# Performance work log

Hardware: AMD Instinct MI355X
Metric: run time of the kernel (lower is better)

The kernel has to match this reference:

```python
import jax, jax.numpy as jnp
from jax import lax
import numpy as np

N_STATE, N_CTRL, T, B = 64, 32, 50, 256
N = N_STATE + N_CTRL


def setup_inputs() -> dict:
    key = jax.random.key(0)
    k1, k2, k3, k4, k5, k6 = jax.random.split(key, 6)
    # SPD cost Hessians so Qt_uu stays invertible through the Riccati recursion
    A = jax.random.normal(k1, (T, B, N, N), jnp.float32) / np.float32(np.sqrt(N))
    C = jnp.einsum('tbij,tbkj->tbik', A, A) + jnp.eye(N, dtype=jnp.float32)
    c = 0.1 * jax.random.normal(k2, (T, B, N), jnp.float32)
    # mildly contractive dynamics to keep the 50-step recursion well-scaled
    F = jax.random.normal(k3, (T, B, N_STATE, N), jnp.float32) * np.float32(0.5 / np.sqrt(N))
    x_init = jax.random.normal(k4, (B, N_STATE), jnp.float32)
    current_x = jax.random.normal(k5, (T, B, N_STATE), jnp.float32)
    current_u = jax.random.normal(k6, (T, B, N_CTRL), jnp.float32)
    return {'x_init': x_init, 'C': C, 'c': c, 'F': F,
            'current_x': current_x, 'current_u': current_u}


def _lqr(x_init, C, c, F, current_x, current_u):
    ns = current_x.shape[-1]
    # delta_space linearized cost: c_back[t] = C[t] @ [x_t; u_t] + c[t]
    xut = jnp.concatenate([current_x, current_u], axis=-1)          # [T,B,N]
    c_back = jnp.einsum('tbij,tbj->tbi', C, xut) + c                # [T,B,N]

    def bwd_step(carry, inp):
        V, v = carry                                                # [B,ns,ns],[B,ns]
        Ct, ct, Ft = inp
        FtT = jnp.swapaxes(Ft, -1, -2)                              # [B,N,ns]
        Qt = Ct + FtT @ V @ Ft                                      # [B,N,N]
        qt = ct + jnp.einsum('bij,bi->bj', Ft, v)                   # Ft^T v
        Q_xx = Qt[:, :ns, :ns]; Q_xu = Qt[:, :ns, ns:]
        Q_ux = Qt[:, ns:, :ns]; Q_uu = Qt[:, ns:, ns:]
        q_x = qt[:, :ns]; q_u = qt[:, ns:]
        Kt = -jnp.linalg.solve(Q_uu, Q_ux)                          # [B,nc,ns]
        kt = -jnp.linalg.solve(Q_uu, q_u[..., None])[..., 0]        # [B,nc]
        KtT = jnp.swapaxes(Kt, -1, -2)
        Vn = Q_xx + Q_xu @ Kt + KtT @ Q_ux + KtT @ Q_uu @ Kt
        vn = (q_x + jnp.einsum('bij,bj->bi', Q_xu, kt)
              + jnp.einsum('bji,bj->bi', Kt, q_u)
              + jnp.einsum('bji,bjk,bk->bi', Kt, Q_uu, kt))
        return (Vn, vn), (Kt, kt)

    Bsz = x_init.shape[0]
    V0 = jnp.zeros((Bsz, ns, ns), C.dtype)
    v0 = jnp.zeros((Bsz, ns), C.dtype)
    # scan from t = T-1 down to 0 (V0 = 0 makes the last step Qt = C[T-1])
    _, (K_rev, k_rev) = lax.scan(bwd_step, (V0, v0),
                                 (C[::-1], c_back[::-1], F[::-1]))
    K = K_rev[::-1]   # [T,B,nc,ns], gain at time t
    k = k_rev[::-1]   # [T,B,nc]

    # forward rollout (single line-search iter, alpha = 1)
    x_ref_next = jnp.concatenate([current_x[1:], jnp.zeros_like(current_x[:1])], 0)

    def fwd_step(carry, inp):
        xt, dxt = carry
        Kt, kt, ut, Ft, xr = inp
        new_ut = jnp.einsum('bij,bj->bi', Kt, dxt) + ut + kt
        new_xut = jnp.concatenate([xt, new_ut], axis=-1)
        x_next = jnp.einsum('bij,bj->bi', Ft, new_xut)
        return (x_next, x_next - xr), (xt, new_ut)

    _, (new_x, new_u) = lax.scan(fwd_step, (x_init, jnp.zeros_like(x_init)),
                                 (K, k, current_u, F, x_ref_next))
    return new_x, new_u


def reference(x_init, C, c, F, current_x, current_u):
    return _lqr(x_init, C, c, F, current_x, current_u)
```

## Files before the change

### kernel.cpp

```cpp
#include <hip/hip_runtime.h>
#include <cstddef>

#define NS 64
#define NC 32
#define NN 96
#define TT 50
#define BB 256
#define NT 512

#define VS 68
#define QS 104
#define FS 104
#define AS 104

#define OFF_V    0
#define OFF_Q    4352
#define OFF_F    14336
#define OFF_M    20992
#define OFF_A    27648
#define OFF_PR   30976
#define OFF_PC   31808
#define OFF_XUT  32064
#define OFF_CV   32160
#define OFF_QT   32256
#define OFF_VV   32352
#define LDS_FLOATS 32416

__device__ __forceinline__ void bar() {
    asm volatile("s_waitcnt lgkmcnt(0)\n\ts_barrier" ::: "memory");
}

__device__ __forceinline__ float frcp(float x) {
    float r = __builtin_amdgcn_rcpf(x);
    return r * (2.f - x * r);
}

extern "C" __global__ __launch_bounds__(NT, 1)
void lqr_fused(const float* __restrict__ x_init,
               const float* __restrict__ Cg, const float* __restrict__ cg,
               const float* __restrict__ Fg, const float* __restrict__ cxg,
               const float* __restrict__ cug, float* __restrict__ Kg,
               float* __restrict__ kg, float* __restrict__ out)
{
    extern __shared__ float sm[];
    float* Vb   = sm + OFF_V;
    float* Qb   = sm + OFF_Q;
    float* Fb   = sm + OFF_F;
    float* Mb   = sm + OFF_M;
    float* Ab   = sm + OFF_A;
    float* PRb  = sm + OFF_PR;
    float* PCb  = sm + OFF_PC;
    float* xut  = sm + OFF_XUT;
    float* cv   = sm + OFF_CV;
    float* qtv  = sm + OFF_QT;
    float* vv   = sm + OFF_VV;

    const int b   = blockIdx.x;
    const int tid = threadIdx.x;

    float4 creg[5];
    float4 fnew[3];
    float  xreg = 0.f, cvreg = 0.f;

    {
        const int t = TT - 1;
        const float* Fsrc = Fg + ((size_t)t * BB + b) * (NS * NN);
        #pragma unroll
        for (int rr = 0; rr < 3; ++rr) {
            int f = tid + NT * rr;
            float4 val = ((const float4*)Fsrc)[f];
            int row = f / 24, c4 = f % 24;
            *(float4*)&Fb[row * FS + 4 * c4] = val;
        }
        const float* Csrc = Cg + ((size_t)t * BB + b) * (NN * NN);
        #pragma unroll
        for (int rr = 0; rr < 4; ++rr) creg[rr] = ((const float4*)Csrc)[tid + NT * rr];
        if (tid < 256) creg[4] = ((const float4*)Csrc)[tid + 2048];

        if (tid < NN) {
            xut[tid] = (tid < NS) ? cxg[((size_t)t * BB + b) * NS + tid]
                                  : cug[((size_t)t * BB + b) * NC + (tid - NS)];
            cv[tid] = cg[((size_t)t * BB + b) * NN + tid];
        }
        for (int e = tid; e < NS * VS; e += NT) Vb[e] = 0.f;
        if (tid < NS) vv[tid] = 0.f;
    }
    bar();

    for (int t = TT - 1; t >= 0; --t) {
        #pragma unroll
        for (int rr = 0; rr < 5; ++rr) {
            if (rr < 4 || tid < 256) {
                int f = tid + NT * rr;
                int row = f / 24, c4 = f % 24;
                *(float4*)&Qb[row * QS + 4 * c4] = creg[rr];
            }
        }
        if (t > 0) {
            const float* Cs = Cg + ((size_t)(t - 1) * BB + b) * (NN * NN);
            #pragma unroll
            for (int rr = 0; rr < 4; ++rr) creg[rr] = ((const float4*)Cs)[tid + NT * rr];
            if (tid < 256) creg[4] = ((const float4*)Cs)[tid + 2048];
            const float* Fs = Fg + ((size_t)(t - 1) * BB + b) * (NS * NN);
            #pragma unroll
            for (int rr = 0; rr < 3; ++rr) fnew[rr] = ((const float4*)Fs)[tid + NT * rr];
            if (tid < NN) {
                xreg  = (tid < NS) ? cxg[((size_t)(t - 1) * BB + b) * NS + tid]
                                   : cug[((size_t)(t - 1) * BB + b) * NC + (tid - NS)];
                cvreg = cg[((size_t)(t - 1) * BB + b) * NN + tid];
            }
        }

        {
            const int ty = tid >> 4, tx = tid & 15;
            const int i0 = 2 * ty, j0 = 6 * tx;
            float acc[2][6];
            #pragma unroll
            for (int a = 0; a < 2; ++a)
                #pragma unroll
                for (int q = 0; q < 6; ++q) acc[a][q] = 0.f;
            for (int k = 0; k < NS; k += 4) {
                float4 v0 = *(const float4*)&Vb[i0 * VS + k];
                float4 v1 = *(const float4*)&Vb[(i0 + 1) * VS + k];
                #pragma unroll
                for (int dk = 0; dk < 4; ++dk) {
                    float2 f0 = *(const float2*)&Fb[(k + dk) * FS + j0];
                    float2 f1 = *(const float2*)&Fb[(k + dk) * FS + j0 + 2];
                    float2 f2 = *(const float2*)&Fb[(k + dk) * FS + j0 + 4];
                    float fv[6] = {f0.x, f0.y, f1.x, f1.y, f2.x, f2.y};
                    float a0k = (&v0.x)[dk], a1k = (&v1.x)[dk];
                    #pragma unroll
                    for (int q = 0; q < 6; ++q) {
                        acc[0][q] += a0k * fv[q];
                        acc[1][q] += a1k * fv[q];
                    }
                }
            }
            #pragma unroll
            for (int a = 0; a < 2; ++a) {
                *(float2*)&Mb[(i0 + a) * FS + j0]     = make_float2(acc[a][0], acc[a][1]);
                *(float2*)&Mb[(i0 + a) * FS + j0 + 2] = make_float2(acc[a][2], acc[a][3]);
                *(float2*)&Mb[(i0 + a) * FS + j0 + 4] = make_float2(acc[a][4], acc[a][5]);
            }
        }
        bar();

        if (tid < 384) {
            const int j = tid >> 2, s = tid & 3;
            float acc = (s == 0) ? cv[j] : 0.f;
            #pragma unroll 4
            for (int it = 0; it < 24; ++it) {
                int i = 4 * it + s;
                acc += Qb[i * QS + j] * xut[i];
            }
            #pragma unroll 4
            for (int it = 0; it < 16; ++it) {
                int i = 4 * it + s;
                acc += Fb[i * FS + j] * vv[i];
            }
            acc += __shfl_down(acc, 1);
            acc += __shfl_down(acc, 2);
            if (s == 0) {
                qtv[j] = acc;
                if (j >= NS) Ab[(j - NS) * AS + 96] = acc;
            }
        }
        bar();

        {
            const int ty = tid >> 4, tx = tid & 15;
            const int a0 = 3 * ty, b0 = 6 * tx;
            float acc[3][6];
            #pragma unroll
            for (int dr = 0; dr < 3; ++dr) {
                float2 q0 = *(const float2*)&Qb[(a0 + dr) * QS + b0];
                float2 q1 = *(const float2*)&Qb[(a0 + dr) * QS + b0 + 2];
                float2 q2 = *(const float2*)&Qb[(a0 + dr) * QS + b0 + 4];
                acc[dr][0] = q0.x; acc[dr][1] = q0.y; acc[dr][2] = q1.x;
                acc[dr][3] = q1.y; acc[dr][4] = q2.x; acc[dr][5] = q2.y;
            }
            for (int i = 0; i < NS; ++i) {
                float fa0 = Fb[i * FS + a0];
                float fa1 = Fb[i * FS + a0 + 1];
                float fa2 = Fb[i * FS + a0 + 2];
                float2 m0 = *(const float2*)&Mb[i * FS + b0];
                float2 m1 = *(const float2*)&Mb[i * FS + b0 + 2];
                float2 m2 = *(const float2*)&Mb[i * FS + b0 + 4];
                float mb[6] = {m0.x, m0.y, m1.x, m1.y, m2.x, m2.y};
                float fa[3] = {fa0, fa1, fa2};
                #pragma unroll
                for (int dr = 0; dr < 3; ++dr)
                    #pragma unroll
                    for (int q = 0; q < 6; ++q) acc[dr][q] += fa[dr] * mb[q];
            }
            #pragma unroll
            for (int dr = 0; dr < 3; ++dr) {
                *(float2*)&Qb[(a0 + dr) * QS + b0]     = make_float2(acc[dr][0], acc[dr][1]);
                *(float2*)&Qb[(a0 + dr) * QS + b0 + 2] = make_float2(acc[dr][2], acc[dr][3]);
                *(float2*)&Qb[(a0 + dr) * QS + b0 + 4] = make_float2(acc[dr][4], acc[dr][5]);
                int row = a0 + dr;
                if (row >= NS) {
                    int rr = row - NS;
                    #pragma unroll
                    for (int q = 0; q < 6; ++q) {
                        int c  = b0 + q;
                        int ac = (c < NS) ? (c + NC) : (c - NS);
                        Ab[rr * AS + ac] = acc[dr][q];
                    }
                }
            }
        }
        bar();

        if (t > 0) {
            #pragma unroll
            for (int rr = 0; rr < 3; ++rr) {
                int f = tid + NT * rr;
                int row = f / 24, c4 = f % 24;
                *(float4*)&Fb[row * FS + 4 * c4] = fnew[rr];
            }
            if (tid < NN) { xut[tid] = xreg; cv[tid] = cvreg; }
        }

        float myinv = 0.f;
        {
            const int g = tid & 15, r = tid >> 4;
            const int jlo = 6 * g;
            float a[6], a6;
            #pragma unroll
            for (int q = 0; q < 6; ++q) a[q] = Ab[r * AS + jlo + q];
            a6 = (g == 15) ? Ab[r * AS + 96] : 0.f;
            if (r < 4) {
                #pragma unroll
                for (int q = 0; q < 6; ++q) PRb[r * 104 + jlo + q] = a[q];
                if (g == 15) PRb[r * 104 + 96] = a6;
            }
            if (g == 0) {
                #pragma unroll
                for (int i = 0; i < 4; ++i) PCb[i * 32 + r] = a[i];
            }
            bar();

            for (int rnd = 0; rnd < 8; ++rnd) {
                const int p0 = 4 * rnd;
                const float* PRc = PRb + (rnd & 1) * 416;
                const float* PCc = PCb + (rnd & 1) * 128;
                float* PRn = PRb + ((rnd + 1) & 1) * 416;
                float* PCn = PCb + ((rnd + 1) & 1) * 128;

                float W0p0 = PRc[0 * 104 + p0 + 0];
                float W0p1 = PRc[0 * 104 + p0 + 1];
                float W0p2 = PRc[0 * 104 + p0 + 2];
                float W0p3 = PRc[0 * 104 + p0 + 3];
                float R1p1 = PRc[1 * 104 + p0 + 1];
                float R1p2 = PRc[1 * 104 + p0 + 2];
                float R1p3 = PRc[1 * 104 + p0 + 3];
                float R2p2 = PRc[2 * 104 + p0 + 2];
                float R2p3 = PRc[2 * 104 + p0 + 3];
                float R3p3 = PRc[3 * 104 + p0 + 3];
                float C0p1 = PCc[0 * 32 + p0 + 1];
                float C0p2 = PCc[0 * 32 + p0 + 2];
                float C0p3 = PCc[0 * 32 + p0 + 3];
                float C1p2 = PCc[1 * 32 + p0 + 2];
                float C1p3 = PCc[1 * 32 + p0 + 3];
                float C2p3 = PCc[2 * 32 + p0 + 3];

                float r0 = frcp(W0p0);
                float g1 = C0p1 * r0;
                float W1p1 = R1p1 - g1 * W0p1;
                float r1 = frcp(W1p1);
                float W1p2 = R1p2 - g1 * W0p2;
                float W1p3 = R1p3 - g1 * W0p3;
                float h0 = C0p2 * r0;
                float h1 = (C1p2 - h0 * W0p1) * r1;
                float W2p2 = R2p2 - h0 * W0p2 - h1 * W1p2;
                float r2 = frcp(W2p2);
                float W2p3 = R2p3 - h0 * W0p3 - h1 * W1p3;
                float k0 = C0p3 * r0;
                float k1 = (C1p3 - k0 * W0p1) * r1;
                float k2 = (C2p3 - k0 * W0p2 - k1 * W1p2) * r2;
                float W3p3 = R3p3 - k0 * W0p3 - k1 * W1p3 - k2 * W2p3;
                float r3 = frcp(W3p3);

                float c0 = PCc[0 * 32 + r];
                float c1 = PCc[1 * 32 + r];
                float c2 = PCc[2 * 32 + r];
                float c3 = PCc[3 * 32 + r];
                float fac0 = (r == p0)     ? 0.f : c0 * r0;
                float a1   = c1 - fac0 * W0p1;
                float fac1 = (r == p0 + 1) ? 0.f : a1 * r1;
                float a2   = c2 - fac0 * W0p2 - fac1 * W1p2;
                float fac2 = (r == p0 + 2) ? 0.f : a2 * r2;
                float a3   = c3 - fac0 * W0p3 - fac1 * W1p3 - fac2 * W2p3;
                float fac3 = (r == p0 + 3) ? 0.f : a3 * r3;

                if (r == p0)     myinv = r0;
                if (r == p0 + 1) myinv = r1;
                if (r == p0 + 2) myinv = r2;
                if (r == p0 + 3) myinv = r3;

                #pragma unroll
                for (int q = 0; q < 6; ++q) {
                    float w0  = PRc[0 * 104 + jlo + q];
                    float w1r = PRc[1 * 104 + jlo + q];
                    float w2r = PRc[2 * 104 + jlo + q];
                    float w3r = PRc[3 * 104 + jlo + q];
                    float w1 = w1r - g1 * w0;
                    float w2 = w2r - h0 * w0 - h1 * w1;
                    float w3 = w3r - k0 * w0 - k1 * w1 - k2 * w2;
                    a[q] -= fac0 * w0;
                    a[q] -= fac1 * w1;
                    a[q] -= fac2 * w2;
                    a[q] -= fac3 * w3;
                }
                if (g == 15) {
                    float w0  = PRc[0 * 104 + 96];
                    float w1 = PRc[1 * 104 + 96] - g1 * w0;
                    float w2 = PRc[2 * 104 + 96] - h0 * w0 - h1 * w1;
                    float w3 = PRc[3 * 104 + 96] - k0 * w0 - k1 * w1 - k2 * w2;
                    a6 -= fac0 * w0;
                    a6 -= fac1 * w1;
                    a6 -= fac2 * w2;
                    a6 -= fac3 * w3;
                }

                if (rnd < 7) {
                    const int np0 = p0 + 4;
                    if (r >= np0 && r < np0 + 4) {
                        float* dst = PRn + (r - np0) * 104;
                        #pragma unroll
                        for (int q = 0; q < 6; ++q) dst[jlo + q] = a[q];
                        if (g == 15) dst[96] = a6;
                    }
                    #pragma unroll
                    for (int q = 0; q < 6; ++q) {
                        int c = jlo + q;
                        if (c >= np0 && c < np0 + 4) PCn[(c - np0) * 32 + r] = a[q];
                    }
                    bar();
                }
            }
            #pragma unroll
            for (int q = 0; q < 6; ++q) {
                int j = jlo + q;
                if (j >= NC) Ab[r * AS + j] = -a[q] * myinv;
            }
            if (g == 15) Ab[r * AS + 96] = -a6 * myinv;
        }
        bar();

        {
            float* Kt = Kg + ((size_t)t * BB + b) * (NC * NS);
            for (int e = tid; e < NC * NS; e += NT) {
                int m = e >> 6, x = e & 63;
                Kt[e] = Ab[m * AS + 32 + x];
            }
            if (tid < NC) kg[((size_t)t * BB + b) * NC + tid] = Ab[tid * AS + 96];
        }
        {
            const int ty = tid >> 4, tx = tid & 15;
            const int i0 = 2 * ty, j0 = 4 * tx;
            float acc[2][4];
            #pragma unroll
            for (int di = 0; di < 2; ++di) {
                float4 q = *(const float4*)&Qb[(i0 + di) * QS + j0];
                acc[di][0] = q.x; acc[di][1] = q.y; acc[di][2] = q.z; acc[di][3] = q.w;
            }
            for (int m = 0; m < NC; ++m) {
                float2 qx = *(const float2*)&Qb[(NS + m) * QS + i0];
                float4 kk = *(const float4*)&Ab[m * AS + 32 + j0];
                float kv[4] = {kk.x, kk.y, kk.z, kk.w};
                #pragma unroll
                for (int dj = 0; dj < 4; ++dj) {
                    acc[0][dj] += qx.x * kv[dj];
                    acc[1][dj] += qx.y * kv[dj];
                }
            }
            #pragma unroll
            for (int di = 0; di < 2; ++di)
                *(float4*)&Vb[(i0 + di) * VS + j0] =
                    make_float4(acc[di][0], acc[di][1], acc[di][2], acc[di][3]);
        }
        if (tid < NS) {
            float s0 = qtv[tid], s1 = 0.f;
            for (int m = 0; m < NC; m += 2) {
                s0 += Qb[(NS + m) * QS + tid] * Ab[m * AS + 96];
                s1 += Qb[(NS + m + 1) * QS + tid] * Ab[(m + 1) * AS + 96];
            }
            vv[tid] = s0 + s1;
        }
        bar();
    }

    asm volatile("s_waitcnt vmcnt(0)" ::: "memory");
    __syncthreads();

    {
        float* xpp = sm;
        float* dxs = sm + 192;
        float* out_x = out;
        float* out_u = out + (size_t)TT * BB * NS;

        if (tid < NS) { xpp[tid] = x_init[(size_t)b * NS + tid]; dxs[tid] = 0.f; }
        bar();

        const int mK = tid >> 3, qK = tid & 7;
        const int iF = tid >> 2, qF = tid & 3;
        float kr[8], fr[24];
        if (tid < 256) {
            const float* Ksrc = Kg + (size_t)b * (NC * NS);
            #pragma unroll
            for (int xx = 0; xx < 8; ++xx) kr[xx] = Ksrc[mK * NS + qK + 8 * xx];
            const float* Fsrc = Fg + (size_t)b * (NS * NN);
            #pragma unroll
            for (int jj = 0; jj < 24; ++jj) fr[jj] = Fsrc[iF * NN + qF + 4 * jj];
        }

        for (int t = 0; t < TT; ++t) {
            const int cur = (t & 1) * 96, nxt = ((t + 1) & 1) * 96;
            const int curd = (t & 1) * 64, nxtd = ((t + 1) & 1) * 64;
            float krn[8], frn[24];
            if (tid < 256) {
                int tn = (t + 1 < TT) ? (t + 1) : t;
                const float* Ksrc = Kg + ((size_t)tn * BB + b) * (NC * NS);
                #pragma unroll
                for (int xx = 0; xx < 8; ++xx) krn[xx] = Ksrc[mK * NS + qK + 8 * xx];
                const float* Fsrc = Fg + ((size_t)tn * BB + b) * (NS * NN);
                #pragma unroll
                for (int jj = 0; jj < 24; ++jj) frn[jj] = Fsrc[iF * NN + qF + 4 * jj];
            }
            if (tid < NS) out_x[((size_t)t * BB + b) * NS + tid] = xpp[cur + tid];
            if (tid < 256) {
                float s = 0.f;
                #pragma unroll
                for (int xx = 0; xx < 8; ++xx) s += kr[xx] * dxs[curd + qK + 8 * xx];
                s += __shfl_down(s, 4); s += __shfl_down(s, 2); s += __shfl_down(s, 1);
                if (qK == 0) {
                    float un = s + cug[((size_t)t * BB + b) * NC + mK]
                                 + kg[((size_t)t * BB + b) * NC + mK];
                    xpp[cur + NS + mK] = un;
                    out_u[((size_t)t * BB + b) * NC + mK] = un;
                }
            }
            bar();
            if (tid < 256) {
                float s = 0.f;
                #pragma unroll
                for (int jj = 0; jj < 24; ++jj) s += fr[jj] * xpp[cur + qF + 4 * jj];
                s += __shfl_down(s, 2); s += __shfl_down(s, 1);
                if (qF == 0) {
                    float xr = (t + 1 < TT) ? cxg[((size_t)(t + 1) * BB + b) * NS + iF] : 0.f;
                    xpp[nxt + iF] = s;
                    dxs[nxtd + iF] = s - xr;
                }
                #pragma unroll
                for (int xx = 0; xx < 8; ++xx) kr[xx] = krn[xx];
                #pragma unroll
                for (int jj = 0; jj < 24; ++jj) fr[jj] = frn[jj];
            }
            bar();
        }
    }
}

extern "C" void kernel_launch(void* const* d_in, const int* in_sizes, int n_in,
                              void* d_out, int out_size, void* d_ws, size_t ws_size,
                              hipStream_t stream)
{
    const float* x_init = (const float*)d_in[0];
    const float* Cg     = (const float*)d_in[1];
    const float* cg     = (const float*)d_in[2];
    const float* Fg     = (const float*)d_in[3];
    const float* cxg    = (const float*)d_in[4];
    const float* cug    = (const float*)d_in[5];
    float* out = (float*)d_out;

    float* Kg = (float*)d_ws;
    float* kg = Kg + (size_t)TT * BB * NC * NS;

    hipFuncSetAttribute((const void*)lqr_fused,
                        hipFuncAttributeMaxDynamicSharedMemorySize,
                        LDS_FLOATS * 4);

    lqr_fused<<<BB, NT, LDS_FLOATS * 4, stream>>>(x_init, Cg, cg, Fg, cxg, cug,
                                                  Kg, kg, out);
}
```

Measured before the change: 1.907 ms.

## Restructure Riccati step with warp-specialized phases, bigger register tiles, skipped pivot work

The backward Riccati step is reorganized in several ways. The V·F matmul now runs on 192 threads with 4x8 tiles, concurrently with the qt reduction on other threads, which removes one barrier. The FᵀM update uses 8x6 tiles with float4 loads and vectorized Ab writes, and the Gauss-Jordan elimination remaps threads so that groups whose columns are already eliminated skip work. It also vectorizes the K store, widens the V update tiles, moves the Q reload to the end of the step, and prefetches the per-step scalars in the forward rollout. The larger tiles raise register pressure and idle part of the block, and the reordered barriers risk correctness hazards.

```diff
diff --git a/kernel.cpp b/kernel.cpp
--- a/kernel.cpp
+++ b/kernel.cpp
@@ -76,18 +76,6 @@
         #pragma unroll
         for (int rr = 0; rr < 4; ++rr) creg[rr] = ((const float4*)Csrc)[tid + NT * rr];
         if (tid < 256) creg[4] = ((const float4*)Csrc)[tid + 2048];
-
-        if (tid < NN) {
-            xut[tid] = (tid < NS) ? cxg[((size_t)t * BB + b) * NS + tid]
-                                  : cug[((size_t)t * BB + b) * NC + (tid - NS)];
-            cv[tid] = cg[((size_t)t * BB + b) * NN + tid];
-        }
-        for (int e = tid; e < NS * VS; e += NT) Vb[e] = 0.f;
-        if (tid < NS) vv[tid] = 0.f;
-    }
-    bar();
-
-    for (int t = TT - 1; t >= 0; --t) {
         #pragma unroll
         for (int rr = 0; rr < 5; ++rr) {
             if (rr < 4 || tid < 256) {
@@ -96,6 +84,17 @@
                 *(float4*)&Qb[row * QS + 4 * c4] = creg[rr];
             }
         }
+        if (tid < NN) {
+            xut[tid] = (tid < NS) ? cxg[((size_t)t * BB + b) * NS + tid]
+                                  : cug[((size_t)t * BB + b) * NC + (tid - NS)];
+            cv[tid] = cg[((size_t)t * BB + b) * NN + tid];
+        }
+        for (int e = tid; e < NS * VS; e += NT) Vb[e] = 0.f;
+        if (tid < NS) vv[tid] = 0.f;
+    }
+    bar();
+
+    for (int t = TT - 1; t >= 0; --t) {
         if (t > 0) {
             const float* Cs = Cg + ((size_t)(t - 1) * BB + b) * (NN * NN);
             #pragma unroll
@@ -111,55 +110,46 @@
             }
         }
 
-        {
-            const int ty = tid >> 4, tx = tid & 15;
-            const int i0 = 2 * ty, j0 = 6 * tx;
-            float acc[2][6];
-            #pragma unroll
-            for (int a = 0; a < 2; ++a)
-                #pragma unroll
-                for (int q = 0; q < 6; ++q) acc[a][q] = 0.f;
+        if (tid < 192) {
+            const int rg = tid & 15;
+            const int cg = tid >> 4;
+            const int j0 = 8 * cg;
+            float acc[4][8];
+            #pragma unroll
+            for (int di = 0; di < 4; ++di)
+                #pragma unroll
+                for (int q = 0; q < 8; ++q) acc[di][q] = 0.f;
             for (int k = 0; k < NS; k += 4) {
-                float4 v0 = *(const float4*)&Vb[i0 * VS + k];
-                float4 v1 = *(const float4*)&Vb[(i0 + 1) * VS + k];
+                float4 v[4];
+                #pragma unroll
+                for (int di = 0; di < 4; ++di)
+                    v[di] = *(const float4*)&Vb[(rg + 16 * di) * VS + k];
                 #pragma unroll
                 for (int dk = 0; dk < 4; ++dk) {
-                    float2 f0 = *(const float2*)&Fb[(k + dk) * FS + j0];
-                    float2 f1 = *(const float2*)&Fb[(k + dk) * FS + j0 + 2];
-                    float2 f2 = *(const float2*)&Fb[(k + dk) * FS + j0 + 4];
-                    float fv[6] = {f0.x, f0.y, f1.x, f1.y, f2.x, f2.y};
-                    float a0k = (&v0.x)[dk], a1k = (&v1.x)[dk];
+                    float4 f0 = *(const float4*)&Fb[(k + dk) * FS + j0];
+                    float4 f1 = *(const float4*)&Fb[(k + dk) * FS + j0 + 4];
+                    float fv[8] = {f0.x, f0.y, f0.z, f0.w, f1.x, f1.y, f1.z, f1.w};
                     #pragma unroll
-                    for (int q = 0; q < 6; ++q) {
-                        acc[0][q] += a0k * fv[q];
-                        acc[1][q] += a1k * fv[q];
+                    for (int di = 0; di < 4; ++di) {
+                        float av = (&v[di].x)[dk];
+                        #pragma unroll
+                        for (int q = 0; q < 8; ++q) acc[di][q] += av * fv[q];
                     }
                 }
             }
             #pragma unroll
-            for (int a = 0; a < 2; ++a) {
-                *(float2*)&Mb[(i0 + a) * FS + j0]     = make_float2(acc[a][0], acc[a][1]);
-                *(float2*)&Mb[(i0 + a) * FS + j0 + 2] = make_float2(acc[a][2], acc[a][3]);
-                *(float2*)&Mb[(i0 + a) * FS + j0 + 4] = make_float2(acc[a][4], acc[a][5]);
-            }
-        }
-        bar();
-
-        if (tid < 384) {
-            const int j = tid >> 2, s = tid & 3;
+            for (int di = 0; di < 4; ++di) {
+                int row = rg + 16 * di;
+                *(float4*)&Mb[row * FS + j0]     = make_float4(acc[di][0], acc[di][1], acc[di][2], acc[di][3]);
+                *(float4*)&Mb[row * FS + j0 + 4] = make_float4(acc[di][4], acc[di][5], acc[di][6], acc[di][7]);
+            }
+        } else if (tid >= 320) {
+            const int u = tid - 320;
+            const int j = u >> 1, s = u & 1;
             float acc = (s == 0) ? cv[j] : 0.f;
-            #pragma unroll 4
-            for (int it = 0; it < 24; ++it) {
-                int i = 4 * it + s;
-                acc += Qb[i * QS + j] * xut[i];
-            }
-            #pragma unroll 4
-            for (int it = 0; it < 16; ++it) {
-                int i = 4 * it + s;
-                acc += Fb[i * FS + j] * vv[i];
-            }
+            for (int i = s; i < NN; i += 2) acc += Qb[i * QS + j] * xut[i];
+            for (int i = s; i < NS; i += 2) acc += Fb[i * FS + j] * vv[i];
             acc += __shfl_down(acc, 1);
-            acc += __shfl_down(acc, 2);
             if (s == 0) {
                 qtv[j] = acc;
                 if (j >= NS) Ab[(j - NS) * AS + 96] = acc;
@@ -167,12 +157,13 @@
         }
         bar();
 
-        {
-            const int ty = tid >> 4, tx = tid & 15;
-            const int a0 = 3 * ty, b0 = 6 * tx;
-            float acc[3][6];
-            #pragma unroll
-            for (int dr = 0; dr < 3; ++dr) {
+        if (tid < 192) {
+            const int ry = tid >> 4;
+            const int tx = tid & 15;
+            const int a0 = 8 * ry, b0 = 6 * tx;
+            float acc[8][6];
+            #pragma unroll
+            for (int dr = 0; dr < 8; ++dr) {
                 float2 q0 = *(const float2*)&Qb[(a0 + dr) * QS + b0];
                 float2 q1 = *(const float2*)&Qb[(a0 + dr) * QS + b0 + 2];
                 float2 q2 = *(const float2*)&Qb[(a0 + dr) * QS + b0 + 4];
@@ -180,32 +171,43 @@
                 acc[dr][3] = q1.y; acc[dr][4] = q2.x; acc[dr][5] = q2.y;
             }
             for (int i = 0; i < NS; ++i) {
-                float fa0 = Fb[i * FS + a0];
-                float fa1 = Fb[i * FS + a0 + 1];
-                float fa2 = Fb[i * FS + a0 + 2];
+                float4 f0 = *(const float4*)&Fb[i * FS + a0];
+                float4 f1 = *(const float4*)&Fb[i * FS + a0 + 4];
                 float2 m0 = *(const float2*)&Mb[i * FS + b0];
                 float2 m1 = *(const float2*)&Mb[i * FS + b0 + 2];
                 float2 m2 = *(const float2*)&Mb[i * FS + b0 + 4];
                 float mb[6] = {m0.x, m0.y, m1.x, m1.y, m2.x, m2.y};
-                float fa[3] = {fa0, fa1, fa2};
-                #pragma unroll
-                for (int dr = 0; dr < 3; ++dr)
+                float fa[8] = {f0.x, f0.y, f0.z, f0.w, f1.x, f1.y, f1.z, f1.w};
+                #pragma unroll
+                for (int dr = 0; dr < 8; ++dr)
                     #pragma unroll
                     for (int q = 0; q < 6; ++q) acc[dr][q] += fa[dr] * mb[q];
             }
             #pragma unroll
-            for (int dr = 0; dr < 3; ++dr) {
+            for (int dr = 0; dr < 8; ++dr) {
                 *(float2*)&Qb[(a0 + dr) * QS + b0]     = make_float2(acc[dr][0], acc[dr][1]);
                 *(float2*)&Qb[(a0 + dr) * QS + b0 + 2] = make_float2(acc[dr][2], acc[dr][3]);
                 *(float2*)&Qb[(a0 + dr) * QS + b0 + 4] = make_float2(acc[dr][4], acc[dr][5]);
-                int row = a0 + dr;
-                if (row >= NS) {
-                    int rr = row - NS;
-                    #pragma unroll
-                    for (int q = 0; q < 6; ++q) {
-                        int c  = b0 + q;
-                        int ac = (c < NS) ? (c + NC) : (c - NS);
-                        Ab[rr * AS + ac] = acc[dr][q];
+            }
+            if (ry >= 8) {
+                #pragma unroll
+                for (int dr = 0; dr < 8; ++dr) {
+                    int rr = a0 + dr - NS;
+                    if (b0 + 5 < NS) {
+                        *(float2*)&Ab[rr * AS + b0 + 32]     = make_float2(acc[dr][0], acc[dr][1]);
+                        *(float2*)&Ab[rr * AS + b0 + 34]     = make_float2(acc[dr][2], acc[dr][3]);
+                        *(float2*)&Ab[rr * AS + b0 + 36]     = make_float2(acc[dr][4], acc[dr][5]);
+                    } else if (b0 >= NS) {
+                        *(float2*)&Ab[rr * AS + b0 - 64]     = make_float2(acc[dr][0], acc[dr][1]);
+                        *(float2*)&Ab[rr * AS + b0 - 62]     = make_float2(acc[dr][2], acc[dr][3]);
+                        *(float2*)&Ab[rr * AS + b0 - 60]     = make_float2(acc[dr][4], acc[dr][5]);
+                    } else {
+                        #pragma unroll
+                        for (int q = 0; q < 6; ++q) {
+                            int c  = b0 + q;
+                            int ac = (c < NS) ? (c + NC) : (c - NS);
+                            Ab[rr * AS + ac] = acc[dr][q];
+                        }
                     }
                 }
             }
@@ -224,7 +226,7 @@
 
         float myinv = 0.f;
         {
-            const int g = tid & 15, r = tid >> 4;
+            const int g = tid >> 5, r = tid & 31;
             const int jlo = 6 * g;
             float a[6], a6;
             #pragma unroll
@@ -247,98 +249,93 @@
                 const float* PCc = PCb + (rnd & 1) * 128;
                 float* PRn = PRb + ((rnd + 1) & 1) * 416;
                 float* PCn = PCb + ((rnd + 1) & 1) * 128;
-
-                float W0p0 = PRc[0 * 104 + p0 + 0];
-                float W0p1 = PRc[0 * 104 + p0 + 1];
-                float W0p2 = PRc[0 * 104 + p0 + 2];
-                float W0p3 = PRc[0 * 104 + p0 + 3];
-                float R1p1 = PRc[1 * 104 + p0 + 1];
-                float R1p2 = PRc[1 * 104 + p0 + 2];
-                float R1p3 = PRc[1 * 104 + p0 + 3];
-                float R2p2 = PRc[2 * 104 + p0 + 2];
-                float R2p3 = PRc[2 * 104 + p0 + 3];
-                float R3p3 = PRc[3 * 104 + p0 + 3];
-                float C0p1 = PCc[0 * 32 + p0 + 1];
-                float C0p2 = PCc[0 * 32 + p0 + 2];
-                float C0p3 = PCc[0 * 32 + p0 + 3];
-                float C1p2 = PCc[1 * 32 + p0 + 2];
-                float C1p3 = PCc[1 * 32 + p0 + 3];
-                float C2p3 = PCc[2 * 32 + p0 + 3];
-
-                float r0 = frcp(W0p0);
-                float g1 = C0p1 * r0;
-                float W1p1 = R1p1 - g1 * W0p1;
-                float r1 = frcp(W1p1);
-                float W1p2 = R1p2 - g1 * W0p2;
-                float W1p3 = R1p3 - g1 * W0p3;
-                float h0 = C0p2 * r0;
-                float h1 = (C1p2 - h0 * W0p1) * r1;
-                float W2p2 = R2p2 - h0 * W0p2 - h1 * W1p2;
-                float r2 = frcp(W2p2);
-                float W2p3 = R2p3 - h0 * W0p3 - h1 * W1p3;
-                float k0 = C0p3 * r0;
-                float k1 = (C1p3 - k0 * W0p1) * r1;
-                float k2 = (C2p3 - k0 * W0p2 - k1 * W1p2) * r2;
-                float W3p3 = R3p3 - k0 * W0p3 - k1 * W1p3 - k2 * W2p3;
-                float r3 = frcp(W3p3);
-
-                float c0 = PCc[0 * 32 + r];
-                float c1 = PCc[1 * 32 + r];
-                float c2 = PCc[2 * 32 + r];
-                float c3 = PCc[3 * 32 + r];
-                float fac0 = (r == p0)     ? 0.f : c0 * r0;
-                float a1   = c1 - fac0 * W0p1;
-                float fac1 = (r == p0 + 1) ? 0.f : a1 * r1;
-                float a2   = c2 - fac0 * W0p2 - fac1 * W1p2;
-                float fac2 = (r == p0 + 2) ? 0.f : a2 * r2;
-                float a3   = c3 - fac0 * W0p3 - fac1 * W1p3 - fac2 * W2p3;
-                float fac3 = (r == p0 + 3) ? 0.f : a3 * r3;
-
-                if (r == p0)     myinv = r0;
-                if (r == p0 + 1) myinv = r1;
-                if (r == p0 + 2) myinv = r2;
-                if (r == p0 + 3) myinv = r3;
-
-                #pragma unroll
-                for (int q = 0; q < 6; ++q) {
-                    float w0  = PRc[0 * 104 + jlo + q];
-                    float w1r = PRc[1 * 104 + jlo + q];
-                    float w2r = PRc[2 * 104 + jlo + q];
-                    float w3r = PRc[3 * 104 + jlo + q];
-                    float w1 = w1r - g1 * w0;
-                    float w2 = w2r - h0 * w0 - h1 * w1;
-                    float w3 = w3r - k0 * w0 - k1 * w1 - k2 * w2;
-                    a[q] -= fac0 * w0;
-                    a[q] -= fac1 * w1;
-                    a[q] -= fac2 * w2;
-                    a[q] -= fac3 * w3;
-                }
-                if (g == 15) {
-                    float w0  = PRc[0 * 104 + 96];
-                    float w1 = PRc[1 * 104 + 96] - g1 * w0;
-                    float w2 = PRc[2 * 104 + 96] - h0 * w0 - h1 * w1;
-                    float w3 = PRc[3 * 104 + 96] - k0 * w0 - k1 * w1 - k2 * w2;
-                    a6 -= fac0 * w0;
-                    a6 -= fac1 * w1;
-                    a6 -= fac2 * w2;
-                    a6 -= fac3 * w3;
-                }
-
-                if (rnd < 7) {
-                    const int np0 = p0 + 4;
-                    if (r >= np0 && r < np0 + 4) {
-                        float* dst = PRn + (r - np0) * 104;
-                        #pragma unroll
-                        for (int q = 0; q < 6; ++q) dst[jlo + q] = a[q];
-                        if (g == 15) dst[96] = a6;
-                    }
+                if (6 * (g | 1) + 5 >= 4 * rnd + 4) {
+                    float4 t0 = *(const float4*)&PRc[0 * 104 + p0];
+                    float4 t1 = *(const float4*)&PRc[1 * 104 + p0];
+                    float4 t2 = *(const float4*)&PRc[2 * 104 + p0];
+                    float4 t3 = *(const float4*)&PRc[3 * 104 + p0];
+                    float C0p1 = PCc[0 * 32 + p0 + 1];
+                    float C0p2 = PCc[0 * 32 + p0 + 2];
+                    float C0p3 = PCc[0 * 32 + p0 + 3];
+                    float C1p2 = PCc[1 * 32 + p0 + 2];
+                    float C1p3 = PCc[1 * 32 + p0 + 3];
+                    float C2p3 = PCc[2 * 32 + p0 + 3];
+
+                    float r0 = frcp(t0.x);
+                    float g1 = C0p1 * r0;
+                    float W1p1 = t1.y - g1 * t0.y;
+                    float r1 = frcp(W1p1);
+                    float W1p2 = t1.z - g1 * t0.z;
+                    float W1p3 = t1.w - g1 * t0.w;
+                    float h0 = C0p2 * r0;
+                    float h1 = (C1p2 - h0 * t0.y) * r1;
+                    float W2p2 = t2.z - h0 * t0.z - h1 * W1p2;
+                    float r2 = frcp(W2p2);
+                    float W2p3 = t2.w - h0 * t0.w - h1 * W1p3;
+                    float k0 = C0p3 * r0;
+                    float k1 = (C1p3 - k0 * t0.y) * r1;
+                    float k2 = (C2p3 - k0 * t0.z - k1 * W1p2) * r2;
+                    float W3p3 = t3.w - k0 * t0.w - k1 * W1p3 - k2 * W2p3;
+                    float r3 = frcp(W3p3);
+
+                    float c0 = PCc[0 * 32 + r];
+                    float c1 = PCc[1 * 32 + r];
+                    float c2 = PCc[2 * 32 + r];
+                    float c3 = PCc[3 * 32 + r];
+                    float fac0 = (r == p0)     ? 0.f : c0 * r0;
+                    float a1v  = c1 - fac0 * t0.y;
+                    float fac1 = (r == p0 + 1) ? 0.f : a1v * r1;
+                    float a2v  = c2 - fac0 * t0.z - fac1 * W1p2;
+                    float fac2 = (r == p0 + 2) ? 0.f : a2v * r2;
+                    float a3v  = c3 - fac0 * t0.w - fac1 * W1p3 - fac2 * W2p3;
+                    float fac3 = (r == p0 + 3) ? 0.f : a3v * r3;
+
+                    if (r == p0)     myinv = r0;
+                    if (r == p0 + 1) myinv = r1;
+                    if (r == p0 + 2) myinv = r2;
+                    if (r == p0 + 3) myinv = r3;
+
                     #pragma unroll
                     for (int q = 0; q < 6; ++q) {
-                        int c = jlo + q;
-                        if (c >= np0 && c < np0 + 4) PCn[(c - np0) * 32 + r] = a[q];
+                        float w0  = PRc[0 * 104 + jlo + q];
+                        float w1r = PRc[1 * 104 + jlo + q];
+                        float w2r = PRc[2 * 104 + jlo + q];
+                        float w3r = PRc[3 * 104 + jlo + q];
+                        float w1 = w1r - g1 * w0;
+                        float w2 = w2r - h0 * w0 - h1 * w1;
+                        float w3 = w3r - k0 * w0 - k1 * w1 - k2 * w2;
+                        a[q] -= fac0 * w0;
+                        a[q] -= fac1 * w1;
+                        a[q] -= fac2 * w2;
+                        a[q] -= fac3 * w3;
                     }
-                    bar();
-                }
+                    if (g == 15) {
+                        float w0 = PRc[0 * 104 + 96];
+                        float w1 = PRc[1 * 104 + 96] - g1 * w0;
+                        float w2 = PRc[2 * 104 + 96] - h0 * w0 - h1 * w1;
+                        float w3 = PRc[3 * 104 + 96] - k0 * w0 - k1 * w1 - k2 * w2;
+                        a6 -= fac0 * w0;
+                        a6 -= fac1 * w1;
+                        a6 -= fac2 * w2;
+                        a6 -= fac3 * w3;
+                    }
+
+                    if (rnd < 7) {
+                        const int np0 = p0 + 4;
+                        if (r >= np0 && r < np0 + 4) {
+                            float* dst = PRn + (r - np0) * 104;
+                            #pragma unroll
+                            for (int q = 0; q < 6; ++q) dst[jlo + q] = a[q];
+                            if (g == 15) dst[96] = a6;
+                        }
+                        #pragma unroll
+                        for (int q = 0; q < 6; ++q) {
+                            int c = jlo + q;
+                            if (c >= np0 && c < np0 + 4) PCn[(c - np0) * 32 + r] = a[q];
+                        }
+                    }
+                }
+                if (rnd < 7) bar();
             }
             #pragma unroll
             for (int q = 0; q < 6; ++q) {
@@ -351,43 +348,54 @@
 
         {
             float* Kt = Kg + ((size_t)t * BB + b) * (NC * NS);
-            for (int e = tid; e < NC * NS; e += NT) {
-                int m = e >> 6, x = e & 63;
-                Kt[e] = Ab[m * AS + 32 + x];
-            }
+            const int m = tid >> 4, xq = tid & 15;
+            float4 kk4 = *(const float4*)&Ab[m * AS + 32 + 4 * xq];
+            *(float4*)&Kt[m * NS + 4 * xq] = kk4;
             if (tid < NC) kg[((size_t)t * BB + b) * NC + tid] = Ab[tid * AS + 96];
         }
-        {
-            const int ty = tid >> 4, tx = tid & 15;
-            const int i0 = 2 * ty, j0 = 4 * tx;
-            float acc[2][4];
-            #pragma unroll
-            for (int di = 0; di < 2; ++di) {
+        if (tid < 256) {
+            const int rg = tid & 15, cg = tid >> 4;
+            const int i0 = 4 * rg, j0 = 4 * cg;
+            float acc[4][4];
+            #pragma unroll
+            for (int di = 0; di < 4; ++di) {
                 float4 q = *(const float4*)&Qb[(i0 + di) * QS + j0];
                 acc[di][0] = q.x; acc[di][1] = q.y; acc[di][2] = q.z; acc[di][3] = q.w;
             }
             for (int m = 0; m < NC; ++m) {
-                float2 qx = *(const float2*)&Qb[(NS + m) * QS + i0];
+                float4 qx = *(const float4*)&Qb[(NS + m) * QS + i0];
                 float4 kk = *(const float4*)&Ab[m * AS + 32 + j0];
                 float kv[4] = {kk.x, kk.y, kk.z, kk.w};
-                #pragma unroll
-                for (int dj = 0; dj < 4; ++dj) {
-                    acc[0][dj] += qx.x * kv[dj];
-                    acc[1][dj] += qx.y * kv[dj];
-                }
-            }
-            #pragma unroll
-            for (int di = 0; di < 2; ++di)
+                float qv[4] = {qx.x, qx.y, qx.z, qx.w};
+                #pragma unroll
+                for (int di = 0; di < 4; ++di)
+                    #pragma unroll
+                    for (int dj = 0; dj < 4; ++dj) acc[di][dj] += qv[di] * kv[dj];
+            }
+            #pragma unroll
+            for (int di = 0; di < 4; ++di)
                 *(float4*)&Vb[(i0 + di) * VS + j0] =
                     make_float4(acc[di][0], acc[di][1], acc[di][2], acc[di][3]);
-        }
-        if (tid < NS) {
-            float s0 = qtv[tid], s1 = 0.f;
+        } else if (tid < 320) {
+            const int x = tid - 256;
+            float s0 = qtv[x], s1 = 0.f;
             for (int m = 0; m < NC; m += 2) {
-                s0 += Qb[(NS + m) * QS + tid] * Ab[m * AS + 96];
-                s1 += Qb[(NS + m + 1) * QS + tid] * Ab[(m + 1) * AS + 96];
-            }
-            vv[tid] = s0 + s1;
+                s0 += Qb[(NS + m) * QS + x] * Ab[m * AS + 96];
+                s1 += Qb[(NS + m + 1) * QS + x] * Ab[(m + 1) * AS + 96];
+            }
+            vv[x] = s0 + s1;
+        }
+        bar();
+
+        if (t > 0) {
+            #pragma unroll
+            for (int rr = 0; rr < 5; ++rr) {
+                if (rr < 4 || tid < 256) {
+                    int f = tid + NT * rr;
+                    int row = f / 24, c4 = f % 24;
+                    *(float4*)&Qb[row * QS + 4 * c4] = creg[rr];
+                }
+            }
         }
         bar();
     }
@@ -407,6 +415,7 @@
         const int mK = tid >> 3, qK = tid & 7;
         const int iF = tid >> 2, qF = tid & 3;
         float kr[8], fr[24];
+        float cu_c = 0.f, kg_c = 0.f, xr_c = 0.f;
         if (tid < 256) {
             const float* Ksrc = Kg + (size_t)b * (NC * NS);
             #pragma unroll
@@ -414,12 +423,17 @@
             const float* Fsrc = Fg + (size_t)b * (NS * NN);
             #pragma unroll
             for (int jj = 0; jj < 24; ++jj) fr[jj] = Fsrc[iF * NN + qF + 4 * jj];
+            if (qK == 0) {
+                cu_c = cug[(size_t)b * NC + mK];
+                kg_c = kg[(size_t)b * NC + mK];
+            }
+            if (qF == 0) xr_c = cxg[((size_t)1 * BB + b) * NS + iF];
         }
 
         for (int t = 0; t < TT; ++t) {
             const int cur = (t & 1) * 96, nxt = ((t + 1) & 1) * 96;
             const int curd = (t & 1) * 64, nxtd = ((t + 1) & 1) * 64;
-            float krn[8], frn[24];
+            float krn[8], frn[24], cu_n = 0.f, kg_n = 0.f, xr_n = 0.f;
             if (tid < 256) {
                 int tn = (t + 1 < TT) ? (t + 1) : t;
                 const float* Ksrc = Kg + ((size_t)tn * BB + b) * (NC * NS);
@@ -428,6 +442,14 @@
                 const float* Fsrc = Fg + ((size_t)tn * BB + b) * (NS * NN);
                 #pragma unroll
                 for (int jj = 0; jj < 24; ++jj) frn[jj] = Fsrc[iF * NN + qF + 4 * jj];
+                if (qK == 0) {
+                    cu_n = cug[((size_t)tn * BB + b) * NC + mK];
+                    kg_n = kg[((size_t)tn * BB + b) * NC + mK];
+                }
+                if (qF == 0) {
+                    int tn2 = (t + 2 < TT) ? (t + 2) : (TT - 1);
+                    xr_n = cxg[((size_t)tn2 * BB + b) * NS + iF];
+                }
             }
             if (tid < NS) out_x[((size_t)t * BB + b) * NS + tid] = xpp[cur + tid];
             if (tid < 256) {
@@ -436,8 +458,7 @@
                 for (int xx = 0; xx < 8; ++xx) s += kr[xx] * dxs[curd + qK + 8 * xx];
                 s += __shfl_down(s, 4); s += __shfl_down(s, 2); s += __shfl_down(s, 1);
                 if (qK == 0) {
-                    float un = s + cug[((size_t)t * BB + b) * NC + mK]
-                                 + kg[((size_t)t * BB + b) * NC + mK];
+                    float un = s + cu_c + kg_c;
                     xpp[cur + NS + mK] = un;
                     out_u[((size_t)t * BB + b) * NC + mK] = un;
                 }
@@ -449,7 +470,7 @@
                 for (int jj = 0; jj < 24; ++jj) s += fr[jj] * xpp[cur + qF + 4 * jj];
                 s += __shfl_down(s, 2); s += __shfl_down(s, 1);
                 if (qF == 0) {
-                    float xr = (t + 1 < TT) ? cxg[((size_t)(t + 1) * BB + b) * NS + iF] : 0.f;
+                    float xr = (t + 1 < TT) ? xr_c : 0.f;
                     xpp[nxt + iF] = s;
                     dxs[nxtd + iF] = s - xr;
                 }
@@ -457,6 +478,7 @@
                 for (int xx = 0; xx < 8; ++xx) kr[xx] = krn[xx];
                 #pragma unroll
                 for (int jj = 0; jj < 24; ++jj) fr[jj] = frn[jj];
+                cu_c = cu_n; kg_c = kg_n; xr_c = xr_n;
             }
             bar();
         }
```

New measurement: 2.150 ms. 1.13x slower.
